# Kernel tuning notes

Measured on AMD Instinct MI355X. Metric: run time of the kernel, lower is better.

The kernel has to match this reference:

```python
import jax, jax.numpy as jnp
import numpy as np

NUM_USERS = 100000
NUM_ITEMS = 50000
NUM_NODES = NUM_USERS + NUM_ITEMS
EMB = 64
NUM_EDGES = 2000000
BATCH = 16384


def setup_inputs() -> dict:
    key = jax.random.key(0)
    ks = jax.random.split(key, 9)

    def xavier(k, shape):
        fan_in, fan_out = shape[-2], shape[-1]
        lim = float(np.sqrt(6.0 / (fan_in + fan_out)))
        return jax.random.uniform(k, shape, jnp.float32, -lim, lim)

    user_table = xavier(ks[0], (NUM_USERS, EMB))
    item_table = xavier(ks[1], (NUM_ITEMS, EMB))
    # gat1: in=64, heads=4, out=64 -> W1 [64, 256]; a1 [4, 128]
    W1 = xavier(ks[2], (EMB, EMB * 4))
    a1 = xavier(ks[3], (4, 2 * EMB))
    # gat2: in=256, heads=1, out=64 -> W2 [256, 64]; a2 [1, 128]
    W2 = xavier(ks[4], (EMB * 4, EMB))
    a2 = xavier(ks[5], (1, 2 * EMB))

    edge_index = jax.random.randint(ks[6], (2, NUM_EDGES), 0, NUM_NODES, dtype=jnp.int32)
    user_ids = jax.random.randint(ks[7], (BATCH,), 0, NUM_USERS, dtype=jnp.int32)
    item_ids = jax.random.randint(ks[8], (BATCH,), 0, NUM_ITEMS, dtype=jnp.int32)
    return {
        "user_table": user_table, "item_table": item_table,
        "W1": W1, "a1": a1, "W2": W2, "a2": a2,
        "edge_index": edge_index, "user_ids": user_ids, "item_ids": item_ids,
    }


def gat_layer(x, W, a, num_heads, out_features, src, dst, concat):
    n = x.shape[0]
    h = (x @ W).reshape(n, num_heads, out_features)          # [N,H,F]
    # attention score: (cat(h_src,h_dst) * a).sum(-1) == h_src.a_l + h_dst.a_r
    a_l, a_r = a[:, :out_features], a[:, out_features:]
    e_src = jnp.einsum('nhf,hf->nh', h, a_l)                 # [N,H]
    e_dst = jnp.einsum('nhf,hf->nh', h, a_r)
    att = e_src[src] + e_dst[dst]                            # [E,H]
    att = jnp.where(att > 0, att, 0.2 * att)                 # LeakyReLU(0.2)
    att = jnp.exp(att - jnp.max(att))                        # global max, as in torch code
    att_sum = jax.ops.segment_sum(att, dst, num_segments=n)  # [N,H]
    att = att / (att_sum[dst] + 1e-8)
    msg = att[:, :, None] * h[src]                           # [E,H,F]
    out = jax.ops.segment_sum(msg, dst, num_segments=n)      # [N,H,F]
    return out.reshape(n, -1) if concat else out.mean(axis=1)


def reference(user_table, item_table, W1, a1, W2, a2, edge_index, user_ids, item_ids):
    src, dst = edge_index[0], edge_index[1]
    all_emb = jnp.concatenate([user_table, item_table], axis=0)  # [N,64]
    h = gat_layer(all_emb, W1, a1, 4, EMB, src, dst, concat=True)  # [N,256]
    h = jax.nn.elu(h)
    h = gat_layer(h, W2, a2, 1, EMB, src, dst, concat=False)       # [N,64]
    h = h + all_emb
    user_emb = h[:NUM_USERS]
    item_emb = h[NUM_USERS:]
    return jnp.sum(user_emb[user_ids] * item_emb[item_ids], axis=1)
```

## Files before the change

kernel.cpp:

```cpp
#include <hip/hip_runtime.h>
#include <cstdint>
#include <cstddef>

#define NUM_USERS 100000
#define NUM_ITEMS 50000
#define NUM_NODES 150000
#define NUM_EDGES 2000000
#define BATCH 16384
#define BSHIFT 8
#define NBUCK ((NUM_NODES + 255) >> BSHIFT)
#define PA_EDGES 8192
#define PA_BLOCKS ((NUM_EDGES + PA_EDGES - 1) / PA_EDGES)
#define NNPAD 150016
#define TBLK2 (NNPAD / 128)
#define AGG_MBLK ((NNPAD + 3) / 4)
#define AGG_SBLK ((NNPAD + 15) / 16)

typedef _Float16 hf8 __attribute__((ext_vector_type(8)));
typedef _Float16 hf4 __attribute__((ext_vector_type(4)));
typedef float fx4 __attribute__((ext_vector_type(4)));

__global__ void flag_kernel(const int* __restrict__ uid, const int* __restrict__ iid,
                            int* __restrict__ nodelist, int* __restrict__ bcnt,
                            int* __restrict__ gcnt,
                            _Float16* __restrict__ aXhi, _Float16* __restrict__ aXlo) {
  int i = blockIdx.x * blockDim.x + threadIdx.x;
  if (i < NBUCK) bcnt[i] = 0;
  if (i < 2) gcnt[i] = 0;
  if (i < 2048) {
    ((float*)(aXhi + (size_t)NUM_NODES * 256))[i] = 0.f;
    ((float*)(aXlo + (size_t)NUM_NODES * 256))[i] = 0.f;
  }
  if (i < BATCH) {
    nodelist[2 * i] = uid[i];
    nodelist[2 * i + 1] = NUM_USERS + iid[i];
  }
}

__global__ __launch_bounds__(256) void bhist_kernel(const int* __restrict__ dst,
                                                    int* __restrict__ bcnt) {
  __shared__ int bh[NBUCK];
  int t = threadIdx.x;
  for (int u = t; u < NBUCK; u += 256) bh[u] = 0;
  __syncthreads();
  int base = blockIdx.x * PA_EDGES;
#pragma unroll
  for (int u = 0; u < PA_EDGES / 256; ++u) {
    int e = base + u * 256 + t;
    if (e < NUM_EDGES) atomicAdd(&bh[dst[e] >> BSHIFT], 1);
  }
  __syncthreads();
  for (int u = t; u < NBUCK; u += 256) {
    int v = bh[u];
    if (v) atomicAdd(&bcnt[u], v);
  }
}

__global__ void bscan_kernel(const int* __restrict__ bcnt, int* __restrict__ bbase,
                             int* __restrict__ bcursor, int* __restrict__ offsets) {
  __shared__ int sh[1024];
  int t = threadIdx.x;
  int v = (t < NBUCK) ? bcnt[t] : 0;
  sh[t] = v;
  __syncthreads();
  for (int off = 1; off < 1024; off <<= 1) {
    int x = (t >= off) ? sh[t - off] : 0;
    __syncthreads();
    sh[t] += x;
    __syncthreads();
  }
  if (t < NBUCK) {
    bbase[t] = sh[t] - v;
    bcursor[t] = sh[t] - v;
  }
  if (t == NBUCK - 1) {
    bbase[NBUCK] = sh[t];
    offsets[NUM_NODES] = sh[t];
  }
}

__global__ __launch_bounds__(256) void bpart_kernel(const int* __restrict__ src,
                                                    const int* __restrict__ dst,
                                                    int* __restrict__ bcursor,
                                                    int2* __restrict__ ebuf) {
  __shared__ int lcnt[NBUCK];
  __shared__ int lbase[NBUCK];
  int t = threadIdx.x;
  for (int u = t; u < NBUCK; u += 256) lcnt[u] = 0;
  __syncthreads();
  int base = blockIdx.x * PA_EDGES;
#pragma unroll
  for (int u = 0; u < PA_EDGES / 256; ++u) {
    int e = base + u * 256 + t;
    if (e < NUM_EDGES) atomicAdd(&lcnt[dst[e] >> BSHIFT], 1);
  }
  __syncthreads();
  for (int u = t; u < NBUCK; u += 256) {
    int v = lcnt[u];
    lbase[u] = v ? atomicAdd(&bcursor[u], v) : 0;
    lcnt[u] = 0;
  }
  __syncthreads();
#pragma unroll
  for (int u = 0; u < PA_EDGES / 256; ++u) {
    int e = base + u * 256 + t;
    if (e < NUM_EDGES) {
      int d = dst[e];
      int b = d >> BSHIFT;
      int p = lbase[b] + atomicAdd(&lcnt[b], 1);
      ebuf[p] = make_int2(src[e], d);
    }
  }
}

__global__ __launch_bounds__(256) void bcsr_kernel(const int2* __restrict__ ebuf,
                                                   const int* __restrict__ bbase,
                                                   int* __restrict__ offsets,
                                                   int* __restrict__ srcs,
                                                   int* __restrict__ gcnt,
                                                   int* __restrict__ Ls,
                                                   int* __restrict__ Lm) {
  __shared__ int ncnt[256];
  __shared__ int sh[256];
  __shared__ int lcur[256];
  __shared__ int c0, c1, b0, b1;
  int b = blockIdx.x;
  int t = threadIdx.x;
  int node0 = b << BSHIFT;
  int ebeg = bbase[b], eend = bbase[b + 1];
  ncnt[t] = 0;
  if (t == 0) { c0 = 0; c1 = 0; }
  __syncthreads();
  for (int i = ebeg + t; i < eend; i += 256)
    atomicAdd(&ncnt[ebuf[i].y - node0], 1);
  __syncthreads();
  int v = ncnt[t];
  sh[t] = v;
  __syncthreads();
  for (int off = 1; off < 256; off <<= 1) {
    int x = (t >= off) ? sh[t - off] : 0;
    __syncthreads();
    sh[t] += x;
    __syncthreads();
  }
  int excl = ebeg + sh[t] - v;
  if (node0 + t < NUM_NODES) offsets[node0 + t] = excl;
  lcur[t] = excl;
  int cls = -1, rank = 0;
  if (node0 + t < NUM_NODES) {
    cls = (v <= 16) ? 0 : 1;
    rank = atomicAdd(cls == 0 ? &c0 : &c1, 1);
  }
  __syncthreads();
  if (t == 0) {
    b0 = atomicAdd(&gcnt[0], c0);
    b1 = atomicAdd(&gcnt[1], c1);
  }
  __syncthreads();
  if (cls == 0) Ls[b0 + rank] = node0 + t;
  else if (cls == 1) Lm[b1 + rank] = node0 + t;
  for (int i = ebeg + t; i < eend; i += 256) {
    int2 ed = ebuf[i];
    int p = atomicAdd(&lcur[ed.y - node0], 1);
    srcs[p] = ed.x;
  }
}

__global__ void prep_kernel(const float* __restrict__ W1, const float* __restrict__ a1,
                            const float* __restrict__ W2,
                            float* __restrict__ w1a, float* __restrict__ w1b,
                            _Float16* __restrict__ w1t_hi, _Float16* __restrict__ w1t_lo,
                            _Float16* __restrict__ w2t_hi, _Float16* __restrict__ w2t_lo) {
  int t = threadIdx.x;
  int h = t >> 6;
  if (blockIdx.x == 0) {
    int k = t & 63;
    float sa = 0.f, sb = 0.f;
    for (int f = 0; f < 64; ++f) {
      float w = W1[(size_t)k * 256 + h * 64 + f];
      sa += w * a1[h * 128 + f];
      sb += w * a1[h * 128 + 64 + f];
    }
    w1a[h * 64 + k] = sa;
    w1b[h * 64 + k] = sb;
  } else {
    int a = t & 63;
    for (int k = 0; k < 64; ++k) {
      float w = W1[(size_t)k * 256 + h * 64 + a] * 256.f;
      _Float16 hi = (_Float16)w;
      w1t_hi[(size_t)(h * 64 + a) * 64 + k] = hi;
      w1t_lo[(size_t)(h * 64 + a) * 64 + k] = (_Float16)(w - (float)hi);
      float v = W2[(size_t)(h * 64 + k) * 64 + a] * 256.f;
      _Float16 hi2 = (_Float16)v;
      w2t_hi[(size_t)(h * 64 + a) * 64 + k] = hi2;
      w2t_lo[(size_t)(h * 64 + a) * 64 + k] = (_Float16)(v - (float)hi2);
    }
  }
}

__device__ __forceinline__ const float* row_ptr(int s, const float* __restrict__ ut,
                                                const float* __restrict__ it) {
  return (s < NUM_USERS) ? ut + (size_t)s * 64 : it + (size_t)(s - NUM_USERS) * 64;
}

__device__ __forceinline__ float lrexp(float x) {
  x = x > 0.f ? x : 0.2f * x;
  return __expf(x);
}

__device__ __forceinline__ float wnorm(float w) {
  float sum = w;
#pragma unroll
  for (int off = 32; off; off >>= 1) sum += __shfl_xor(sum, off, 64);
  return w * (1.f / (sum + 1e-8f));
}

__device__ __forceinline__ void fold4(float4& a) {
#pragma unroll
  for (int off = 16; off <= 32; off <<= 1) {
    a.x += __shfl_xor(a.x, off, 64);
    a.y += __shfl_xor(a.y, off, 64);
    a.z += __shfl_xor(a.z, off, 64);
    a.w += __shfl_xor(a.w, off, 64);
  }
}

__device__ __forceinline__ float elu(float x) {
  return x > 0.f ? x : (__expf(x) - 1.f);
}

__device__ __forceinline__ void split4(float4 o, hf4& hv, hf4& lv) {
  float a0 = o.x * 256.f, a1 = o.y * 256.f, a2 = o.z * 256.f, a3 = o.w * 256.f;
  _Float16 h0 = (_Float16)a0, h1 = (_Float16)a1;
  _Float16 h2 = (_Float16)a2, h3 = (_Float16)a3;
  hv[0] = h0; hv[1] = h1; hv[2] = h2; hv[3] = h3;
  lv[0] = (_Float16)(a0 - (float)h0);
  lv[1] = (_Float16)(a1 - (float)h1);
  lv[2] = (_Float16)(a2 - (float)h2);
  lv[3] = (_Float16)(a3 - (float)h3);
}

__device__ __forceinline__ void splitstore(_Float16* __restrict__ hi,
                                           _Float16* __restrict__ lo,
                                           size_t idx, float v) {
  v *= 256.f;
  _Float16 h = (_Float16)v;
  hi[idx] = h;
  lo[idx] = (_Float16)(v - (float)h);
}

__global__ __launch_bounds__(256) void e1g_kernel(
    const float* __restrict__ ut, const float* __restrict__ it,
    const float* __restrict__ w1a, const float* __restrict__ w1b,
    float* __restrict__ e1s, float* __restrict__ e1d) {
  int t = threadIdx.x;
  int wave = t >> 6, lane = t & 63;
  int g = lane >> 4, fl = lane & 15;
  int node = blockIdx.x * 16 + wave * 4 + g;
  bool valid = node < NUM_NODES;
  float4 xv = make_float4(0.f, 0.f, 0.f, 0.f);
  if (valid) xv = *(const float4*)(row_ptr(node, ut, it) + fl * 4);
  float ps[4], pd[4];
#pragma unroll
  for (int h = 0; h < 4; ++h) {
    float4 wa = *(const float4*)(w1a + h * 64 + fl * 4);
    float4 wb = *(const float4*)(w1b + h * 64 + fl * 4);
    ps[h] = xv.x * wa.x + xv.y * wa.y + xv.z * wa.z + xv.w * wa.w;
    pd[h] = xv.x * wb.x + xv.y * wb.y + xv.z * wb.z + xv.w * wb.w;
  }
#pragma unroll
  for (int off = 8; off; off >>= 1) {
#pragma unroll
    for (int h = 0; h < 4; ++h) {
      ps[h] += __shfl_xor(ps[h], off, 16);
      pd[h] += __shfl_xor(pd[h], off, 16);
    }
  }
  if (valid && fl == 0) {
    *(float4*)(e1s + (size_t)node * 4) = make_float4(ps[0], ps[1], ps[2], ps[3]);
    *(float4*)(e1d + (size_t)node * 4) = make_float4(pd[0], pd[1], pd[2], pd[3]);
  }
}

__global__ __launch_bounds__(256) void aggX_kernel(
    const int* __restrict__ Ls, const int* __restrict__ Lm,
    const int* __restrict__ gcnt,
    const int* __restrict__ offsets, const int* __restrict__ srcs,
    const float* __restrict__ e1s, const float* __restrict__ e1d,
    const float* __restrict__ ut, const float* __restrict__ it,
    _Float16* __restrict__ aXhi, _Float16* __restrict__ aXlo) {
  __shared__ int sS[4][68];
  __shared__ __align__(16) float4 sW[4][68];
  const int t = threadIdx.x;
  const int wave = t >> 6, lane = t & 63;
  const int g = lane >> 4, fl = lane & 15;

  if (blockIdx.x < AGG_MBLK) {
    int idx = blockIdx.x * 4 + wave;
    if (idx >= gcnt[1]) return;
    int node = Lm[idx];
    int beg = offsets[node], end = offsets[node + 1];
    int deg = end - beg;

    float edv0 = e1d[(size_t)node * 4 + 0];
    float edv1 = e1d[(size_t)node * 4 + 1];
    float edv2 = e1d[(size_t)node * 4 + 2];
    float edv3 = e1d[(size_t)node * 4 + 3];

    if (deg <= 64) {
      int s = 0;
      float w0 = 0.f, w1 = 0.f, w2 = 0.f, w3 = 0.f;
      if (lane < deg) {
        s = srcs[beg + lane];
        float4 ev = *(const float4*)(e1s + (size_t)s * 4);
        w0 = lrexp(ev.x + edv0);
        w1 = lrexp(ev.y + edv1);
        w2 = lrexp(ev.z + edv2);
        w3 = lrexp(ev.w + edv3);
      }
      w0 = wnorm(w0);
      w1 = wnorm(w1);
      w2 = wnorm(w2);
      w3 = wnorm(w3);

      float4 acc0 = make_float4(0.f, 0.f, 0.f, 0.f);
      float4 acc1 = acc0, acc2 = acc0, acc3 = acc0;
      for (int ebase = 0; ebase < deg; ebase += 16) {
        int i0 = ebase + g, i1 = ebase + 4 + g, i2 = ebase + 8 + g, i3 = ebase + 12 + g;
        int s0 = __shfl(s, i0, 64), s1 = __shfl(s, i1, 64);
        int s2 = __shfl(s, i2, 64), s3 = __shfl(s, i3, 64);
        float4 x0 = *(const float4*)(row_ptr(s0, ut, it) + fl * 4);
        float4 x1 = *(const float4*)(row_ptr(s1, ut, it) + fl * 4);
        float4 x2 = *(const float4*)(row_ptr(s2, ut, it) + fl * 4);
        float4 x3 = *(const float4*)(row_ptr(s3, ut, it) + fl * 4);
#pragma unroll
        for (int j = 0; j < 4; ++j) {
          int ei = ebase + j * 4 + g;
          float4 xv = (j == 0) ? x0 : (j == 1) ? x1 : (j == 2) ? x2 : x3;
          float wg0 = __shfl(w0, ei, 64);
          acc0.x += wg0 * xv.x; acc0.y += wg0 * xv.y;
          acc0.z += wg0 * xv.z; acc0.w += wg0 * xv.w;
          float wg1 = __shfl(w1, ei, 64);
          acc1.x += wg1 * xv.x; acc1.y += wg1 * xv.y;
          acc1.z += wg1 * xv.z; acc1.w += wg1 * xv.w;
          float wg2 = __shfl(w2, ei, 64);
          acc2.x += wg2 * xv.x; acc2.y += wg2 * xv.y;
          acc2.z += wg2 * xv.z; acc2.w += wg2 * xv.w;
          float wg3 = __shfl(w3, ei, 64);
          acc3.x += wg3 * xv.x; acc3.y += wg3 * xv.y;
          acc3.z += wg3 * xv.z; acc3.w += wg3 * xv.w;
        }
      }
      fold4(acc0); fold4(acc1); fold4(acc2); fold4(acc3);

      float4 o = (g == 0) ? acc0 : (g == 1) ? acc1 : (g == 2) ? acc2 : acc3;
      hf4 hv, lv;
      split4(o, hv, lv);
      *(hf4*)(aXhi + (size_t)node * 256 + lane * 4) = hv;
      *(hf4*)(aXlo + (size_t)node * 256 + lane * 4) = lv;
    } else {
      float s0 = 0.f, s1 = 0.f, s2 = 0.f, s3 = 0.f;
      for (int e = beg + lane; e < end; e += 64) {
        int s = srcs[e];
        float4 ev = *(const float4*)(e1s + (size_t)s * 4);
        s0 += lrexp(ev.x + edv0); s1 += lrexp(ev.y + edv1);
        s2 += lrexp(ev.z + edv2); s3 += lrexp(ev.w + edv3);
      }
#pragma unroll
      for (int off = 32; off; off >>= 1) {
        s0 += __shfl_xor(s0, off, 64);
        s1 += __shfl_xor(s1, off, 64);
        s2 += __shfl_xor(s2, off, 64);
        s3 += __shfl_xor(s3, off, 64);
      }
      float i0 = 1.f / (s0 + 1e-8f), i1 = 1.f / (s1 + 1e-8f);
      float i2 = 1.f / (s2 + 1e-8f), i3 = 1.f / (s3 + 1e-8f);
      float a0 = 0.f, a1 = 0.f, a2 = 0.f, a3 = 0.f;
      for (int e = beg; e < end; ++e) {
        int sn = srcs[e];
        float xv = row_ptr(sn, ut, it)[lane];
        float4 ev = *(const float4*)(e1s + (size_t)sn * 4);
        a0 += lrexp(ev.x + edv0) * i0 * xv;
        a1 += lrexp(ev.y + edv1) * i1 * xv;
        a2 += lrexp(ev.z + edv2) * i2 * xv;
        a3 += lrexp(ev.w + edv3) * i3 * xv;
      }
      splitstore(aXhi, aXlo, (size_t)node * 256 + 0 * 64 + lane, a0);
      splitstore(aXhi, aXlo, (size_t)node * 256 + 1 * 64 + lane, a1);
      splitstore(aXhi, aXlo, (size_t)node * 256 + 2 * 64 + lane, a2);
      splitstore(aXhi, aXlo, (size_t)node * 256 + 3 * 64 + lane, a3);
    }
    return;
  }

  const int cnt = gcnt[0];
  const int widx = (blockIdx.x - AGG_MBLK) * 16 + wave * 4 + g;
  const int node = (widx < cnt) ? Ls[widx] : -1;

  int beg = 0, deg = 0;
  float4 ed = make_float4(0.f, 0.f, 0.f, 0.f);
  if (node >= 0) {
    beg = offsets[node];
    deg = offsets[node + 1] - beg;
    ed = *(const float4*)(e1d + (size_t)node * 4);
  }
  int s = 0;
  float w0 = 0.f, w1 = 0.f, w2 = 0.f, w3 = 0.f;
  if (fl < deg) {
    s = srcs[beg + fl];
    float4 ev = *(const float4*)(e1s + (size_t)s * 4);
    w0 = lrexp(ev.x + ed.x);
    w1 = lrexp(ev.y + ed.y);
    w2 = lrexp(ev.z + ed.z);
    w3 = lrexp(ev.w + ed.w);
  }
  float t0 = w0, t1 = w1, t2 = w2, t3 = w3;
#pragma unroll
  for (int off = 8; off; off >>= 1) {
    t0 += __shfl_xor(t0, off, 16);
    t1 += __shfl_xor(t1, off, 16);
    t2 += __shfl_xor(t2, off, 16);
    t3 += __shfl_xor(t3, off, 16);
  }
  w0 *= 1.f / (t0 + 1e-8f);
  w1 *= 1.f / (t1 + 1e-8f);
  w2 *= 1.f / (t2 + 1e-8f);
  w3 *= 1.f / (t3 + 1e-8f);
  sS[wave][g * 17 + fl] = s;
  sW[wave][g * 17 + fl] = make_float4(w0, w1, w2, w3);

  float4 xr[16];
#pragma unroll
  for (int e = 0; e < 16; ++e) {
    int se = sS[wave][g * 17 + e];
    xr[e] = *(const float4*)(row_ptr(se, ut, it) + fl * 4);
  }

  float4 a0 = make_float4(0.f, 0.f, 0.f, 0.f);
  float4 a1 = a0, a2 = a0, a3 = a0;
#pragma unroll
  for (int e = 0; e < 16; ++e) {
    float4 w4 = sW[wave][g * 17 + e];
    float4 xv = xr[e];
    a0.x += w4.x * xv.x; a0.y += w4.x * xv.y; a0.z += w4.x * xv.z; a0.w += w4.x * xv.w;
    a1.x += w4.y * xv.x; a1.y += w4.y * xv.y; a1.z += w4.y * xv.z; a1.w += w4.y * xv.w;
    a2.x += w4.z * xv.x; a2.y += w4.z * xv.y; a2.z += w4.z * xv.z; a2.w += w4.z * xv.w;
    a3.x += w4.w * xv.x; a3.y += w4.w * xv.y; a3.z += w4.w * xv.z; a3.w += w4.w * xv.w;
  }
  if (node >= 0) {
    hf4 hv, lv;
    split4(a0, hv, lv);
    *(hf4*)(aXhi + (size_t)node * 256 + 0 * 64 + fl * 4) = hv;
    *(hf4*)(aXlo + (size_t)node * 256 + 0 * 64 + fl * 4) = lv;
    split4(a1, hv, lv);
    *(hf4*)(aXhi + (size_t)node * 256 + 1 * 64 + fl * 4) = hv;
    *(hf4*)(aXlo + (size_t)node * 256 + 1 * 64 + fl * 4) = lv;
    split4(a2, hv, lv);
    *(hf4*)(aXhi + (size_t)node * 256 + 2 * 64 + fl * 4) = hv;
    *(hf4*)(aXlo + (size_t)node * 256 + 2 * 64 + fl * 4) = lv;
    split4(a3, hv, lv);
    *(hf4*)(aXhi + (size_t)node * 256 + 3 * 64 + fl * 4) = hv;
    *(hf4*)(aXlo + (size_t)node * 256 + 3 * 64 + fl * 4) = lv;
  }
}

__device__ __forceinline__ fx4 mfma3(fx4 c, hf8 ah, hf8 al, hf8 bh, hf8 bl) {
  c = __builtin_amdgcn_mfma_f32_16x16x32_f16(ah, bh, c, 0, 0, 0);
  c = __builtin_amdgcn_mfma_f32_16x16x32_f16(al, bh, c, 0, 0, 0);
  c = __builtin_amdgcn_mfma_f32_16x16x32_f16(ah, bl, c, 0, 0, 0);
  return c;
}

__global__ __launch_bounds__(256, 2) void trans_mfma_kernel(
    const _Float16* __restrict__ aXhi, const _Float16* __restrict__ aXlo,
    const _Float16* __restrict__ w1t_hi, const _Float16* __restrict__ w1t_lo,
    const _Float16* __restrict__ w2t_hi, const _Float16* __restrict__ w2t_lo,
    const float* __restrict__ a2v,
    float* __restrict__ h2g, float* __restrict__ e2s, float* __restrict__ e2d) {
  __shared__ __align__(16) _Float16 t1hi[4][32 * 64];
  __shared__ __align__(16) _Float16 t1lo[4][32 * 64];
  const int wave = threadIdx.x >> 6;
  const int l = threadIdx.x & 63;
  const int lr = l & 15, lg = l >> 4;
  const int node0 = (blockIdx.x * 4 + wave) * 32;
  char* myhi = (char*)&t1hi[wave][0];
  char* mylo = (char*)&t1lo[wave][0];
  const float DS = 1.52587890625e-05f;

  const size_t xbase0 = (size_t)(node0 + 0 * 16 + lr) * 256 + lg * 8;
  const size_t xbase1 = (size_t)(node0 + 1 * 16 + lr) * 256 + lg * 8;

  fx4 acc2[4][2];
#pragma unroll
  for (int m = 0; m < 4; ++m)
#pragma unroll
    for (int n = 0; n < 2; ++n) acc2[m][n] = (fx4){0.f, 0.f, 0.f, 0.f};

  hf8 cxh[4], cxl[4];
#pragma unroll
  for (int ks = 0; ks < 2; ++ks) {
    cxh[ks * 2 + 0] = *(const hf8*)(aXhi + xbase0 + ks * 32);
    cxl[ks * 2 + 0] = *(const hf8*)(aXlo + xbase0 + ks * 32);
    cxh[ks * 2 + 1] = *(const hf8*)(aXhi + xbase1 + ks * 32);
    cxl[ks * 2 + 1] = *(const hf8*)(aXlo + xbase1 + ks * 32);
  }

#pragma unroll
  for (int h = 0; h < 4; ++h) {
    fx4 acc1[4][2];
#pragma unroll
    for (int m = 0; m < 4; ++m)
#pragma unroll
      for (int n = 0; n < 2; ++n) acc1[m][n] = (fx4){0.f, 0.f, 0.f, 0.f};

#pragma unroll
    for (int ks = 0; ks < 2; ++ks) {
      const int ko = ks * 32 + lg * 8;
#pragma unroll
      for (int m = 0; m < 4; ++m) {
        size_t wo = (size_t)((h * 64 + m * 16 + lr) * 64 + ko);
        hf8 wah = *(const hf8*)(w1t_hi + wo);
        hf8 wal = *(const hf8*)(w1t_lo + wo);
#pragma unroll
        for (int n = 0; n < 2; ++n)
          acc1[m][n] = mfma3(acc1[m][n], wah, wal, cxh[ks * 2 + n], cxl[ks * 2 + n]);
      }
    }

    if (h < 3) {
#pragma unroll
      for (int ks = 0; ks < 2; ++ks) {
        cxh[ks * 2 + 0] = *(const hf8*)(aXhi + xbase0 + (h + 1) * 64 + ks * 32);
        cxl[ks * 2 + 0] = *(const hf8*)(aXlo + xbase0 + (h + 1) * 64 + ks * 32);
        cxh[ks * 2 + 1] = *(const hf8*)(aXhi + xbase1 + (h + 1) * 64 + ks * 32);
        cxl[ks * 2 + 1] = *(const hf8*)(aXlo + xbase1 + (h + 1) * 64 + ks * 32);
      }
    }

#pragma unroll
    for (int m = 0; m < 4; ++m)
#pragma unroll
      for (int n = 0; n < 2; ++n) {
        hf4 hv, lv;
#pragma unroll
        for (int r = 0; r < 4; ++r) {
          float v = acc1[m][n][r] * DS;
          v = elu(v) * 256.f;
          _Float16 hi = (_Float16)v;
          hv[r] = hi;
          lv[r] = (_Float16)(v - (float)hi);
        }
        int nl = n * 16 + lr;
        int ro = (m * 32 + lg * 8) ^ ((nl & 7) << 4);
        *(hf4*)(myhi + nl * 128 + ro) = hv;
        *(hf4*)(mylo + nl * 128 + ro) = lv;
      }

#pragma unroll
    for (int ks = 0; ks < 2; ++ks) {
      const int ko = ks * 32 + lg * 8;
      hf8 tbh[2], tbl[2];
#pragma unroll
      for (int n = 0; n < 2; ++n) {
        int nl = n * 16 + lr;
        int ro = (ks * 64 + lg * 16) ^ ((nl & 7) << 4);
        tbh[n] = *(const hf8*)(myhi + nl * 128 + ro);
        tbl[n] = *(const hf8*)(mylo + nl * 128 + ro);
      }
#pragma unroll
      for (int m = 0; m < 4; ++m) {
        size_t wo = (size_t)((h * 64 + m * 16 + lr) * 64 + ko);
        hf8 wah = *(const hf8*)(w2t_hi + wo);
        hf8 wal = *(const hf8*)(w2t_lo + wo);
#pragma unroll
        for (int n = 0; n < 2; ++n)
          acc2[m][n] = mfma3(acc2[m][n], wah, wal, tbh[n], tbl[n]);
      }
    }
  }

  float ps[2] = {0.f, 0.f};
  float pd[2] = {0.f, 0.f};
#pragma unroll
  for (int m = 0; m < 4; ++m) {
    fx4 al = *(const fx4*)(a2v + m * 16 + lg * 4);
    fx4 ar = *(const fx4*)(a2v + 64 + m * 16 + lg * 4);
#pragma unroll
    for (int n = 0; n < 2; ++n) {
      fx4 v = acc2[m][n] * DS;
      int node = node0 + n * 16 + lr;
      if (node < NUM_NODES)
        *(fx4*)(h2g + (size_t)node * 64 + m * 16 + lg * 4) = v;
      ps[n] += v[0] * al[0] + v[1] * al[1] + v[2] * al[2] + v[3] * al[3];
      pd[n] += v[0] * ar[0] + v[1] * ar[1] + v[2] * ar[2] + v[3] * ar[3];
    }
  }
#pragma unroll
  for (int n = 0; n < 2; ++n) {
    float s = ps[n], d = pd[n];
    s += __shfl_xor(s, 16, 64);
    s += __shfl_xor(s, 32, 64);
    d += __shfl_xor(d, 16, 64);
    d += __shfl_xor(d, 32, 64);
    int node = node0 + n * 16 + lr;
    if (lg == n && node < NUM_NODES) {
      e2s[node] = s;
      e2d[node] = d;
    }
  }
}

__global__ __launch_bounds__(256) void agg2_kernel(
    const int* __restrict__ offsets, const int* __restrict__ srcs,
    const float* __restrict__ e2s, const float* __restrict__ e2d,
    const int* __restrict__ nodelist, const float* __restrict__ h2,
    const float* __restrict__ ut, const float* __restrict__ it,
    float* __restrict__ hfin) {
  int wid = threadIdx.x >> 6, lane = threadIdx.x & 63;
  int idx = blockIdx.x * 4 + wid;
  if (idx >= 2 * BATCH) return;
  int node = nodelist[idx];
  int beg = offsets[node], end = offsets[node + 1];
  int deg = end - beg;
  float edv = e2d[node];

  if (deg <= 64) {
    int s = 0;
    float w = 0.f;
    if (lane < deg) {
      s = srcs[beg + lane];
      w = lrexp(e2s[s] + edv);
    }
    w = wnorm(w);

    const int g = lane >> 4, fl = lane & 15;
    float4 acc = make_float4(0.f, 0.f, 0.f, 0.f);
#pragma unroll 4
    for (int e = 0; e < deg; e += 4) {
      int ei = e + g;
      int sg = __shfl(s, ei, 64);
      float wg = __shfl(w, ei, 64);
      float4 hv = *(const float4*)(h2 + (size_t)sg * 64 + fl * 4);
      acc.x += wg * hv.x; acc.y += wg * hv.y; acc.z += wg * hv.z; acc.w += wg * hv.w;
    }
    fold4(acc);
    if (g == 0) {
      const float* rp = (node < NUM_USERS) ? ut + (size_t)node * 64
                                           : it + (size_t)(node - NUM_USERS) * 64;
      float4 res = *(const float4*)(rp + fl * 4);
      acc.x += res.x; acc.y += res.y; acc.z += res.z; acc.w += res.w;
      *(float4*)(hfin + (size_t)node * 64 + fl * 4) = acc;
    }
  } else {
    float psum = 0.f;
    for (int e = beg + lane; e < end; e += 64) {
      int s = srcs[e];
      psum += lrexp(e2s[s] + edv);
    }
#pragma unroll
    for (int off = 32; off; off >>= 1) psum += __shfl_xor(psum, off, 64);
    float inv = 1.f / (psum + 1e-8f);
    float acc = 0.f;
    for (int e = beg; e < end; ++e) {
      int s0 = srcs[e];
      acc += lrexp(e2s[s0] + edv) * inv * h2[(size_t)s0 * 64 + lane];
    }
    float res = (node < NUM_USERS) ? ut[(size_t)node * 64 + lane]
                                   : it[(size_t)(node - NUM_USERS) * 64 + lane];
    hfin[(size_t)node * 64 + lane] = acc + res;
  }
}

__global__ __launch_bounds__(256) void final_kernel(
    const float* __restrict__ hf, const int* __restrict__ uid,
    const int* __restrict__ iid, float* __restrict__ out) {
  int wid = threadIdx.x >> 6, lane = threadIdx.x & 63;
  int idx = blockIdx.x * 4 + wid;
  if (idx >= BATCH) return;
  int u = uid[idx], v = iid[idx];
  float a = hf[(size_t)u * 64 + lane];
  float b = hf[(size_t)(NUM_USERS + v) * 64 + lane];
  float p = a * b;
#pragma unroll
  for (int off = 32; off; off >>= 1) p += __shfl_xor(p, off, 64);
  if (lane == 0) out[idx] = p;
}

extern "C" void kernel_launch(void* const* d_in, const int* in_sizes, int n_in,
                              void* d_out, int out_size, void* d_ws, size_t ws_size,
                              hipStream_t stream) {
  const float* user_table = (const float*)d_in[0];
  const float* item_table = (const float*)d_in[1];
  const float* W1 = (const float*)d_in[2];
  const float* a1 = (const float*)d_in[3];
  const float* W2 = (const float*)d_in[4];
  const float* a2 = (const float*)d_in[5];
  const int* edge_index = (const int*)d_in[6];
  const int* user_ids = (const int*)d_in[7];
  const int* item_ids = (const int*)d_in[8];
  float* out = (float*)d_out;

  const int* src = edge_index;
  const int* dst = edge_index + NUM_EDGES;

  float* ws = (float*)d_ws;
  size_t off = 0;
  auto falloc = [&](size_t n) { float* p = ws + off; off += n; return p; };
  float* h2  = falloc((size_t)NUM_NODES * 64);
  float* e1s = falloc((size_t)NUM_NODES * 4);
  float* e1d = falloc((size_t)NUM_NODES * 4);
  float* e2s = falloc(NUM_NODES);
  float* e2d = falloc(NUM_NODES);
  float* w1a = falloc(256);
  float* w1b = falloc(256);
  int* offsets  = (int*)falloc(NUM_NODES + 1);
  int* srcs     = (int*)falloc(NUM_EDGES);
  int* nodelist = (int*)falloc(2 * BATCH);
  int* bcnt     = (int*)falloc(NBUCK);
  int* bbase    = (int*)falloc(NBUCK + 1);
  int* bcursor  = (int*)falloc(NBUCK);
  int* gcnt     = (int*)falloc(2);
  int* Ls       = (int*)falloc(NNPAD);
  int* Lm       = (int*)falloc(NNPAD);
  off = (off + 3) & ~(size_t)3;
  _Float16* aggXhi = (_Float16*)(ws + off); off += (size_t)NNPAD * 128;
  _Float16* aggXlo = (_Float16*)(ws + off); off += (size_t)NNPAD * 128;

  int2* ebuf = (int2*)aggXhi;
  float* hfin = (float*)aggXhi;
  _Float16* w1t_hi = (_Float16*)falloc(4 * 64 * 64 / 2 + 16);
  _Float16* w1t_lo = (_Float16*)falloc(4 * 64 * 64 / 2 + 16);
  _Float16* w2t_hi = (_Float16*)falloc(4 * 64 * 64 / 2 + 16);
  _Float16* w2t_lo = (_Float16*)falloc(4 * 64 * 64 / 2 + 16);

  flag_kernel<<<(BATCH + 255) / 256, 256, 0, stream>>>(user_ids, item_ids,
                                                       nodelist, bcnt, gcnt,
                                                       aggXhi, aggXlo);
  bhist_kernel<<<PA_BLOCKS, 256, 0, stream>>>(dst, bcnt);
  bscan_kernel<<<1, 1024, 0, stream>>>(bcnt, bbase, bcursor, offsets);
  bpart_kernel<<<PA_BLOCKS, 256, 0, stream>>>(src, dst, bcursor, ebuf);
  bcsr_kernel<<<NBUCK, 256, 0, stream>>>(ebuf, bbase, offsets, srcs,
                                         gcnt, Ls, Lm);

  prep_kernel<<<2, 256, 0, stream>>>(W1, a1, W2, w1a, w1b,
                                     w1t_hi, w1t_lo, w2t_hi, w2t_lo);
  e1g_kernel<<<(NNPAD + 15) / 16, 256, 0, stream>>>(user_table, item_table,
                                                    w1a, w1b, e1s, e1d);

  aggX_kernel<<<AGG_MBLK + AGG_SBLK, 256, 0, stream>>>(Ls, Lm, gcnt, offsets, srcs,
                                                       e1s, e1d, user_table,
                                                       item_table, aggXhi, aggXlo);
  trans_mfma_kernel<<<TBLK2, 256, 0, stream>>>(aggXhi, aggXlo,
                                               w1t_hi, w1t_lo, w2t_hi, w2t_lo,
                                               a2, h2, e2s, e2d);

  agg2_kernel<<<(2 * BATCH + 3) / 4, 256, 0, stream>>>(offsets, srcs, e2s, e2d,
                                                       nodelist, h2,
                                                       user_table, item_table, hfin);
  final_kernel<<<(BATCH + 3) / 4, 256, 0, stream>>>(hfin, user_ids, item_ids, out);
}
```

Before: 489.4 us.

## Merge setup/prep, fuse e1 scoring into CSR build, fuse agg2 with final dot

```diff
diff --git a/kernel.cpp b/kernel.cpp
--- a/kernel.cpp
+++ b/kernel.cpp
@@ -15,165 +15,32 @@
 #define TBLK2 (NNPAD / 128)
 #define AGG_MBLK ((NNPAD + 3) / 4)
 #define AGG_SBLK ((NNPAD + 15) / 16)
+#define E1_BLK ((NNPAD + 15) / 16)
 
 typedef _Float16 hf8 __attribute__((ext_vector_type(8)));
 typedef _Float16 hf4 __attribute__((ext_vector_type(4)));
 typedef float fx4 __attribute__((ext_vector_type(4)));
 
-__global__ void flag_kernel(const int* __restrict__ uid, const int* __restrict__ iid,
-                            int* __restrict__ nodelist, int* __restrict__ bcnt,
-                            int* __restrict__ gcnt,
-                            _Float16* __restrict__ aXhi, _Float16* __restrict__ aXlo) {
-  int i = blockIdx.x * blockDim.x + threadIdx.x;
-  if (i < NBUCK) bcnt[i] = 0;
-  if (i < 2) gcnt[i] = 0;
-  if (i < 2048) {
-    ((float*)(aXhi + (size_t)NUM_NODES * 256))[i] = 0.f;
-    ((float*)(aXlo + (size_t)NUM_NODES * 256))[i] = 0.f;
-  }
-  if (i < BATCH) {
-    nodelist[2 * i] = uid[i];
-    nodelist[2 * i + 1] = NUM_USERS + iid[i];
-  }
-}
-
-__global__ __launch_bounds__(256) void bhist_kernel(const int* __restrict__ dst,
-                                                    int* __restrict__ bcnt) {
-  __shared__ int bh[NBUCK];
+__global__ void setup_kernel(const float* __restrict__ W1, const float* __restrict__ a1,
+                             const float* __restrict__ W2,
+                             int* __restrict__ bcnt, int* __restrict__ gcnt,
+                             _Float16* __restrict__ aXhi, _Float16* __restrict__ aXlo,
+                             float* __restrict__ w1a, float* __restrict__ w1b,
+                             _Float16* __restrict__ w1t_hi, _Float16* __restrict__ w1t_lo,
+                             _Float16* __restrict__ w2t_hi, _Float16* __restrict__ w2t_lo) {
   int t = threadIdx.x;
-  for (int u = t; u < NBUCK; u += 256) bh[u] = 0;
-  __syncthreads();
-  int base = blockIdx.x * PA_EDGES;
-#pragma unroll
-  for (int u = 0; u < PA_EDGES / 256; ++u) {
-    int e = base + u * 256 + t;
-    if (e < NUM_EDGES) atomicAdd(&bh[dst[e] >> BSHIFT], 1);
-  }
-  __syncthreads();
-  for (int u = t; u < NBUCK; u += 256) {
-    int v = bh[u];
-    if (v) atomicAdd(&bcnt[u], v);
-  }
-}
-
-__global__ void bscan_kernel(const int* __restrict__ bcnt, int* __restrict__ bbase,
-                             int* __restrict__ bcursor, int* __restrict__ offsets) {
-  __shared__ int sh[1024];
-  int t = threadIdx.x;
-  int v = (t < NBUCK) ? bcnt[t] : 0;
-  sh[t] = v;
-  __syncthreads();
-  for (int off = 1; off < 1024; off <<= 1) {
-    int x = (t >= off) ? sh[t - off] : 0;
-    __syncthreads();
-    sh[t] += x;
-    __syncthreads();
-  }
-  if (t < NBUCK) {
-    bbase[t] = sh[t] - v;
-    bcursor[t] = sh[t] - v;
-  }
-  if (t == NBUCK - 1) {
-    bbase[NBUCK] = sh[t];
-    offsets[NUM_NODES] = sh[t];
-  }
-}
-
-__global__ __launch_bounds__(256) void bpart_kernel(const int* __restrict__ src,
-                                                    const int* __restrict__ dst,
-                                                    int* __restrict__ bcursor,
-                                                    int2* __restrict__ ebuf) {
-  __shared__ int lcnt[NBUCK];
-  __shared__ int lbase[NBUCK];
-  int t = threadIdx.x;
-  for (int u = t; u < NBUCK; u += 256) lcnt[u] = 0;
-  __syncthreads();
-  int base = blockIdx.x * PA_EDGES;
-#pragma unroll
-  for (int u = 0; u < PA_EDGES / 256; ++u) {
-    int e = base + u * 256 + t;
-    if (e < NUM_EDGES) atomicAdd(&lcnt[dst[e] >> BSHIFT], 1);
-  }
-  __syncthreads();
-  for (int u = t; u < NBUCK; u += 256) {
-    int v = lcnt[u];
-    lbase[u] = v ? atomicAdd(&bcursor[u], v) : 0;
-    lcnt[u] = 0;
-  }
-  __syncthreads();
-#pragma unroll
-  for (int u = 0; u < PA_EDGES / 256; ++u) {
-    int e = base + u * 256 + t;
-    if (e < NUM_EDGES) {
-      int d = dst[e];
-      int b = d >> BSHIFT;
-      int p = lbase[b] + atomicAdd(&lcnt[b], 1);
-      ebuf[p] = make_int2(src[e], d);
-    }
-  }
-}
-
-__global__ __launch_bounds__(256) void bcsr_kernel(const int2* __restrict__ ebuf,
-                                                   const int* __restrict__ bbase,
-                                                   int* __restrict__ offsets,
-                                                   int* __restrict__ srcs,
-                                                   int* __restrict__ gcnt,
-                                                   int* __restrict__ Ls,
-                                                   int* __restrict__ Lm) {
-  __shared__ int ncnt[256];
-  __shared__ int sh[256];
-  __shared__ int lcur[256];
-  __shared__ int c0, c1, b0, b1;
-  int b = blockIdx.x;
-  int t = threadIdx.x;
-  int node0 = b << BSHIFT;
-  int ebeg = bbase[b], eend = bbase[b + 1];
-  ncnt[t] = 0;
-  if (t == 0) { c0 = 0; c1 = 0; }
-  __syncthreads();
-  for (int i = ebeg + t; i < eend; i += 256)
-    atomicAdd(&ncnt[ebuf[i].y - node0], 1);
-  __syncthreads();
-  int v = ncnt[t];
-  sh[t] = v;
-  __syncthreads();
-  for (int off = 1; off < 256; off <<= 1) {
-    int x = (t >= off) ? sh[t - off] : 0;
-    __syncthreads();
-    sh[t] += x;
-    __syncthreads();
-  }
-  int excl = ebeg + sh[t] - v;
-  if (node0 + t < NUM_NODES) offsets[node0 + t] = excl;
-  lcur[t] = excl;
-  int cls = -1, rank = 0;
-  if (node0 + t < NUM_NODES) {
-    cls = (v <= 16) ? 0 : 1;
-    rank = atomicAdd(cls == 0 ? &c0 : &c1, 1);
-  }
-  __syncthreads();
-  if (t == 0) {
-    b0 = atomicAdd(&gcnt[0], c0);
-    b1 = atomicAdd(&gcnt[1], c1);
-  }
-  __syncthreads();
-  if (cls == 0) Ls[b0 + rank] = node0 + t;
-  else if (cls == 1) Lm[b1 + rank] = node0 + t;
-  for (int i = ebeg + t; i < eend; i += 256) {
-    int2 ed = ebuf[i];
-    int p = atomicAdd(&lcur[ed.y - node0], 1);
-    srcs[p] = ed.x;
-  }
-}
-
-__global__ void prep_kernel(const float* __restrict__ W1, const float* __restrict__ a1,
-                            const float* __restrict__ W2,
-                            float* __restrict__ w1a, float* __restrict__ w1b,
-                            _Float16* __restrict__ w1t_hi, _Float16* __restrict__ w1t_lo,
-                            _Float16* __restrict__ w2t_hi, _Float16* __restrict__ w2t_lo) {
-  int t = threadIdx.x;
+  if (blockIdx.x < 8) {
+    int i = blockIdx.x * 256 + t;
+    if (i < NBUCK) bcnt[i] = 0;
+    if (i < 2) gcnt[i] = 0;
+    if (i < 2048) {
+      ((float*)(aXhi + (size_t)NUM_NODES * 256))[i] = 0.f;
+      ((float*)(aXlo + (size_t)NUM_NODES * 256))[i] = 0.f;
+    }
+    return;
+  }
   int h = t >> 6;
-  if (blockIdx.x == 0) {
+  if (blockIdx.x == 8) {
     int k = t & 63;
     float sa = 0.f, sb = 0.f;
     for (int f = 0; f < 64; ++f) {
@@ -198,9 +65,169 @@
   }
 }
 
+__global__ __launch_bounds__(256) void bhist_kernel(const int* __restrict__ dst,
+                                                    int* __restrict__ bcnt) {
+  __shared__ int bh[NBUCK];
+  int t = threadIdx.x;
+  for (int u = t; u < NBUCK; u += 256) bh[u] = 0;
+  __syncthreads();
+  int base = blockIdx.x * PA_EDGES;
+#pragma unroll
+  for (int u = 0; u < PA_EDGES / 256; ++u) {
+    int e = base + u * 256 + t;
+    if (e < NUM_EDGES) atomicAdd(&bh[dst[e] >> BSHIFT], 1);
+  }
+  __syncthreads();
+  for (int u = t; u < NBUCK; u += 256) {
+    int v = bh[u];
+    if (v) atomicAdd(&bcnt[u], v);
+  }
+}
+
+__global__ void bscan_kernel(const int* __restrict__ bcnt, int* __restrict__ bbase,
+                             int* __restrict__ bcursor, int* __restrict__ offsets) {
+  __shared__ int sh[1024];
+  int t = threadIdx.x;
+  int v = (t < NBUCK) ? bcnt[t] : 0;
+  sh[t] = v;
+  __syncthreads();
+  for (int off = 1; off < 1024; off <<= 1) {
+    int x = (t >= off) ? sh[t - off] : 0;
+    __syncthreads();
+    sh[t] += x;
+    __syncthreads();
+  }
+  if (t < NBUCK) {
+    bbase[t] = sh[t] - v;
+    bcursor[t] = sh[t] - v;
+  }
+  if (t == NBUCK - 1) {
+    bbase[NBUCK] = sh[t];
+    offsets[NUM_NODES] = sh[t];
+  }
+}
+
+__global__ __launch_bounds__(256) void bpart_kernel(const int* __restrict__ src,
+                                                    const int* __restrict__ dst,
+                                                    int* __restrict__ bcursor,
+                                                    int2* __restrict__ ebuf) {
+  __shared__ int lcnt[NBUCK];
+  __shared__ int lbase[NBUCK];
+  int t = threadIdx.x;
+  for (int u = t; u < NBUCK; u += 256) lcnt[u] = 0;
+  __syncthreads();
+  int base = blockIdx.x * PA_EDGES;
+#pragma unroll
+  for (int u = 0; u < PA_EDGES / 256; ++u) {
+    int e = base + u * 256 + t;
+    if (e < NUM_EDGES) atomicAdd(&lcnt[dst[e] >> BSHIFT], 1);
+  }
+  __syncthreads();
+  for (int u = t; u < NBUCK; u += 256) {
+    int v = lcnt[u];
+    lbase[u] = v ? atomicAdd(&bcursor[u], v) : 0;
+    lcnt[u] = 0;
+  }
+  __syncthreads();
+#pragma unroll
+  for (int u = 0; u < PA_EDGES / 256; ++u) {
+    int e = base + u * 256 + t;
+    if (e < NUM_EDGES) {
+      int d = dst[e];
+      int b = d >> BSHIFT;
+      int p = lbase[b] + atomicAdd(&lcnt[b], 1);
+      ebuf[p] = make_int2(src[e], d);
+    }
+  }
+}
+
 __device__ __forceinline__ const float* row_ptr(int s, const float* __restrict__ ut,
                                                 const float* __restrict__ it) {
   return (s < NUM_USERS) ? ut + (size_t)s * 64 : it + (size_t)(s - NUM_USERS) * 64;
+}
+
+__global__ __launch_bounds__(256) void bcsr_e1_kernel(
+    const int2* __restrict__ ebuf, const int* __restrict__ bbase,
+    int* __restrict__ offsets, int* __restrict__ srcs,
+    int* __restrict__ gcnt, int* __restrict__ Ls, int* __restrict__ Lm,
+    const float* __restrict__ ut, const float* __restrict__ it,
+    const float* __restrict__ w1a, const float* __restrict__ w1b,
+    float* __restrict__ e1s, float* __restrict__ e1d) {
+  __shared__ int ncnt[256];
+  __shared__ int sh[256];
+  __shared__ int lcur[256];
+  __shared__ int c0, c1, b0, b1;
+  int t = threadIdx.x;
+
+  if (blockIdx.x >= NBUCK) {
+    int wave = t >> 6, lane = t & 63;
+    int g = lane >> 4, fl = lane & 15;
+    int node = (blockIdx.x - NBUCK) * 16 + wave * 4 + g;
+    bool valid = node < NUM_NODES;
+    float4 xv = make_float4(0.f, 0.f, 0.f, 0.f);
+    if (valid) xv = *(const float4*)(row_ptr(node, ut, it) + fl * 4);
+    float ps[4], pd[4];
+#pragma unroll
+    for (int h = 0; h < 4; ++h) {
+      float4 wa = *(const float4*)(w1a + h * 64 + fl * 4);
+      float4 wb = *(const float4*)(w1b + h * 64 + fl * 4);
+      ps[h] = xv.x * wa.x + xv.y * wa.y + xv.z * wa.z + xv.w * wa.w;
+      pd[h] = xv.x * wb.x + xv.y * wb.y + xv.z * wb.z + xv.w * wb.w;
+    }
+#pragma unroll
+    for (int off = 8; off; off >>= 1) {
+#pragma unroll
+      for (int h = 0; h < 4; ++h) {
+        ps[h] += __shfl_xor(ps[h], off, 16);
+        pd[h] += __shfl_xor(pd[h], off, 16);
+      }
+    }
+    if (valid && fl == 0) {
+      *(float4*)(e1s + (size_t)node * 4) = make_float4(ps[0], ps[1], ps[2], ps[3]);
+      *(float4*)(e1d + (size_t)node * 4) = make_float4(pd[0], pd[1], pd[2], pd[3]);
+    }
+    return;
+  }
+
+  int b = blockIdx.x;
+  int node0 = b << BSHIFT;
+  int ebeg = bbase[b], eend = bbase[b + 1];
+  ncnt[t] = 0;
+  if (t == 0) { c0 = 0; c1 = 0; }
+  __syncthreads();
+  for (int i = ebeg + t; i < eend; i += 256)
+    atomicAdd(&ncnt[ebuf[i].y - node0], 1);
+  __syncthreads();
+  int v = ncnt[t];
+  sh[t] = v;
+  __syncthreads();
+  for (int off = 1; off < 256; off <<= 1) {
+    int x = (t >= off) ? sh[t - off] : 0;
+    __syncthreads();
+    sh[t] += x;
+    __syncthreads();
+  }
+  int excl = ebeg + sh[t] - v;
+  if (node0 + t < NUM_NODES) offsets[node0 + t] = excl;
+  lcur[t] = excl;
+  int cls = -1, rank = 0;
+  if (node0 + t < NUM_NODES) {
+    cls = (v <= 16) ? 0 : 1;
+    rank = atomicAdd(cls == 0 ? &c0 : &c1, 1);
+  }
+  __syncthreads();
+  if (t == 0) {
+    b0 = atomicAdd(&gcnt[0], c0);
+    b1 = atomicAdd(&gcnt[1], c1);
+  }
+  __syncthreads();
+  if (cls == 0) Ls[b0 + rank] = node0 + t;
+  else if (cls == 1) Lm[b1 + rank] = node0 + t;
+  for (int i = ebeg + t; i < eend; i += 256) {
+    int2 ed = ebuf[i];
+    int p = atomicAdd(&lcur[ed.y - node0], 1);
+    srcs[p] = ed.x;
+  }
 }
 
 __device__ __forceinline__ float lrexp(float x) {
@@ -247,39 +274,6 @@
   _Float16 h = (_Float16)v;
   hi[idx] = h;
   lo[idx] = (_Float16)(v - (float)h);
-}
-
-__global__ __launch_bounds__(256) void e1g_kernel(
-    const float* __restrict__ ut, const float* __restrict__ it,
-    const float* __restrict__ w1a, const float* __restrict__ w1b,
-    float* __restrict__ e1s, float* __restrict__ e1d) {
-  int t = threadIdx.x;
-  int wave = t >> 6, lane = t & 63;
-  int g = lane >> 4, fl = lane & 15;
-  int node = blockIdx.x * 16 + wave * 4 + g;
-  bool valid = node < NUM_NODES;
-  float4 xv = make_float4(0.f, 0.f, 0.f, 0.f);
-  if (valid) xv = *(const float4*)(row_ptr(node, ut, it) + fl * 4);
-  float ps[4], pd[4];
-#pragma unroll
-  for (int h = 0; h < 4; ++h) {
-    float4 wa = *(const float4*)(w1a + h * 64 + fl * 4);
-    float4 wb = *(const float4*)(w1b + h * 64 + fl * 4);
-    ps[h] = xv.x * wa.x + xv.y * wa.y + xv.z * wa.z + xv.w * wa.w;
-    pd[h] = xv.x * wb.x + xv.y * wb.y + xv.z * wb.z + xv.w * wb.w;
-  }
-#pragma unroll
-  for (int off = 8; off; off >>= 1) {
-#pragma unroll
-    for (int h = 0; h < 4; ++h) {
-      ps[h] += __shfl_xor(ps[h], off, 16);
-      pd[h] += __shfl_xor(pd[h], off, 16);
-    }
-  }
-  if (valid && fl == 0) {
-    *(float4*)(e1s + (size_t)node * 4) = make_float4(ps[0], ps[1], ps[2], ps[3]);
-    *(float4*)(e1d + (size_t)node * 4) = make_float4(pd[0], pd[1], pd[2], pd[3]);
-  }
 }
 
 __global__ __launch_bounds__(256) void aggX_kernel(
@@ -610,19 +604,16 @@
   }
 }
 
-__global__ __launch_bounds__(256) void agg2_kernel(
-    const int* __restrict__ offsets, const int* __restrict__ srcs,
+__device__ __forceinline__ float4 agg2_node(
+    int node, const int* __restrict__ offsets, const int* __restrict__ srcs,
     const float* __restrict__ e2s, const float* __restrict__ e2d,
-    const int* __restrict__ nodelist, const float* __restrict__ h2,
-    const float* __restrict__ ut, const float* __restrict__ it,
-    float* __restrict__ hfin) {
-  int wid = threadIdx.x >> 6, lane = threadIdx.x & 63;
-  int idx = blockIdx.x * 4 + wid;
-  if (idx >= 2 * BATCH) return;
-  int node = nodelist[idx];
+    const float* __restrict__ h2, const float* __restrict__ ut,
+    const float* __restrict__ it, int lane, int g, int fl) {
   int beg = offsets[node], end = offsets[node + 1];
   int deg = end - beg;
   float edv = e2d[node];
+  const float* rp = (node < NUM_USERS) ? ut + (size_t)node * 64
+                                       : it + (size_t)(node - NUM_USERS) * 64;
 
   if (deg <= 64) {
     int s = 0;
@@ -632,8 +623,6 @@
       w = lrexp(e2s[s] + edv);
     }
     w = wnorm(w);
-
-    const int g = lane >> 4, fl = lane & 15;
     float4 acc = make_float4(0.f, 0.f, 0.f, 0.f);
 #pragma unroll 4
     for (int e = 0; e < deg; e += 4) {
@@ -644,13 +633,9 @@
       acc.x += wg * hv.x; acc.y += wg * hv.y; acc.z += wg * hv.z; acc.w += wg * hv.w;
     }
     fold4(acc);
-    if (g == 0) {
-      const float* rp = (node < NUM_USERS) ? ut + (size_t)node * 64
-                                           : it + (size_t)(node - NUM_USERS) * 64;
-      float4 res = *(const float4*)(rp + fl * 4);
-      acc.x += res.x; acc.y += res.y; acc.z += res.z; acc.w += res.w;
-      *(float4*)(hfin + (size_t)node * 64 + fl * 4) = acc;
-    }
+    float4 res = *(const float4*)(rp + fl * 4);
+    acc.x += res.x; acc.y += res.y; acc.z += res.z; acc.w += res.w;
+    return acc;
   } else {
     float psum = 0.f;
     for (int e = beg + lane; e < end; e += 64) {
@@ -665,25 +650,34 @@
       int s0 = srcs[e];
       acc += lrexp(e2s[s0] + edv) * inv * h2[(size_t)s0 * 64 + lane];
     }
-    float res = (node < NUM_USERS) ? ut[(size_t)node * 64 + lane]
-                                   : it[(size_t)(node - NUM_USERS) * 64 + lane];
-    hfin[(size_t)node * 64 + lane] = acc + res;
-  }
-}
-
-__global__ __launch_bounds__(256) void final_kernel(
-    const float* __restrict__ hf, const int* __restrict__ uid,
-    const int* __restrict__ iid, float* __restrict__ out) {
+    acc += rp[lane];
+    float4 r;
+    r.x = __shfl(acc, fl * 4 + 0, 64);
+    r.y = __shfl(acc, fl * 4 + 1, 64);
+    r.z = __shfl(acc, fl * 4 + 2, 64);
+    r.w = __shfl(acc, fl * 4 + 3, 64);
+    return r;
+  }
+}
+
+__global__ __launch_bounds__(256) void agg2f_kernel(
+    const int* __restrict__ offsets, const int* __restrict__ srcs,
+    const float* __restrict__ e2s, const float* __restrict__ e2d,
+    const int* __restrict__ uid, const int* __restrict__ iid,
+    const float* __restrict__ h2, const float* __restrict__ ut,
+    const float* __restrict__ it, float* __restrict__ out) {
   int wid = threadIdx.x >> 6, lane = threadIdx.x & 63;
   int idx = blockIdx.x * 4 + wid;
   if (idx >= BATCH) return;
-  int u = uid[idx], v = iid[idx];
-  float a = hf[(size_t)u * 64 + lane];
-  float b = hf[(size_t)(NUM_USERS + v) * 64 + lane];
-  float p = a * b;
-#pragma unroll
-  for (int off = 32; off; off >>= 1) p += __shfl_xor(p, off, 64);
-  if (lane == 0) out[idx] = p;
+  const int g = lane >> 4, fl = lane & 15;
+  int u = uid[idx];
+  int v = NUM_USERS + iid[idx];
+  float4 ru = agg2_node(u, offsets, srcs, e2s, e2d, h2, ut, it, lane, g, fl);
+  float4 rv = agg2_node(v, offsets, srcs, e2s, e2d, h2, ut, it, lane, g, fl);
+  float pr = ru.x * rv.x + ru.y * rv.y + ru.z * rv.z + ru.w * rv.w;
+#pragma unroll
+  for (int off = 8; off; off >>= 1) pr += __shfl_xor(pr, off, 16);
+  if (lane == 0) out[idx] = pr;
 }
 
 extern "C" void kernel_launch(void* const* d_in, const int* in_sizes, int n_in,
@@ -715,7 +709,6 @@
   float* w1b = falloc(256);
   int* offsets  = (int*)falloc(NUM_NODES + 1);
   int* srcs     = (int*)falloc(NUM_EDGES);
-  int* nodelist = (int*)falloc(2 * BATCH);
   int* bcnt     = (int*)falloc(NBUCK);
   int* bbase    = (int*)falloc(NBUCK + 1);
   int* bcursor  = (int*)falloc(NBUCK);
@@ -727,25 +720,20 @@
   _Float16* aggXlo = (_Float16*)(ws + off); off += (size_t)NNPAD * 128;
 
   int2* ebuf = (int2*)aggXhi;
-  float* hfin = (float*)aggXhi;
   _Float16* w1t_hi = (_Float16*)falloc(4 * 64 * 64 / 2 + 16);
   _Float16* w1t_lo = (_Float16*)falloc(4 * 64 * 64 / 2 + 16);
   _Float16* w2t_hi = (_Float16*)falloc(4 * 64 * 64 / 2 + 16);
   _Float16* w2t_lo = (_Float16*)falloc(4 * 64 * 64 / 2 + 16);
 
-  flag_kernel<<<(BATCH + 255) / 256, 256, 0, stream>>>(user_ids, item_ids,
-                                                       nodelist, bcnt, gcnt,
-                                                       aggXhi, aggXlo);
+  setup_kernel<<<10, 256, 0, stream>>>(W1, a1, W2, bcnt, gcnt, aggXhi, aggXlo,
+                                       w1a, w1b, w1t_hi, w1t_lo, w2t_hi, w2t_lo);
   bhist_kernel<<<PA_BLOCKS, 256, 0, stream>>>(dst, bcnt);
   bscan_kernel<<<1, 1024, 0, stream>>>(bcnt, bbase, bcursor, offsets);
   bpart_kernel<<<PA_BLOCKS, 256, 0, stream>>>(src, dst, bcursor, ebuf);
-  bcsr_kernel<<<NBUCK, 256, 0, stream>>>(ebuf, bbase, offsets, srcs,
-                                         gcnt, Ls, Lm);
-
-  prep_kernel<<<2, 256, 0, stream>>>(W1, a1, W2, w1a, w1b,
-                                     w1t_hi, w1t_lo, w2t_hi, w2t_lo);
-  e1g_kernel<<<(NNPAD + 15) / 16, 256, 0, stream>>>(user_table, item_table,
-                                                    w1a, w1b, e1s, e1d);
+  bcsr_e1_kernel<<<NBUCK + E1_BLK, 256, 0, stream>>>(ebuf, bbase, offsets, srcs,
+                                                     gcnt, Ls, Lm,
+                                                     user_table, item_table,
+                                                     w1a, w1b, e1s, e1d);
 
   aggX_kernel<<<AGG_MBLK + AGG_SBLK, 256, 0, stream>>>(Ls, Lm, gcnt, offsets, srcs,
                                                        e1s, e1d, user_table,
@@ -754,8 +742,7 @@
                                                w1t_hi, w1t_lo, w2t_hi, w2t_lo,
                                                a2, h2, e2s, e2d);
 
-  agg2_kernel<<<(2 * BATCH + 3) / 4, 256, 0, stream>>>(offsets, srcs, e2s, e2d,
-                                                       nodelist, h2,
-                                                       user_table, item_table, hfin);
-  final_kernel<<<(BATCH + 3) / 4, 256, 0, stream>>>(hfin, user_ids, item_ids, out);
-}
+  agg2f_kernel<<<(BATCH + 3) / 4, 256, 0, stream>>>(offsets, srcs, e2s, e2d,
+                                                    user_ids, item_ids, h2,
+                                                    user_table, item_table, out);
+}
```

Measured after the change: 468.4 us. -4.3%, faster.
